# Kernel tuning notes

Measured on AMD Instinct MI355X. Metric: run time of the kernel, lower is better.

The kernel has to match this reference:

```python
import jax, jax.numpy as jnp
import numpy as np

ALPHA = 0.2  # LeakyReLU negative slope
NEG = -9e15  # mask value from original code


def setup_inputs() -> dict:
    key = jax.random.key(0)
    k1, k2, k3, k4 = jax.random.split(key, 4)
    N, F_in, F_out = 8192, 256, 128
    h = jax.random.normal(k1, (N, F_in), dtype=jnp.float32)
    adj = jax.random.randint(k2, (N, N), 0, 2, dtype=jnp.int32)
    # xavier-ish scaled params
    W = jax.random.normal(k3, (F_out, F_in), dtype=jnp.float32) * (1.0 / np.sqrt(F_in))
    a = jax.random.normal(k4, (1, 2 * F_out), dtype=jnp.float32) * (1.0 / np.sqrt(2 * F_out))
    return {"h": h, "adj": adj, "W": W, "a": a}


def reference(h, adj, W, a):
    # Wh: [N, F_out]
    Wh = h @ W.T
    F_out = Wh.shape[1]
    # Algebraic decomposition of the pairwise-concat score:
    # e[i,j] = leakyrelu(a . [Wh_i ; Wh_j]) = leakyrelu(f1_i + f2_j)
    a1 = a[0, :F_out]   # [F_out]
    a2 = a[0, F_out:]   # [F_out]
    f1 = Wh @ a1        # [N]
    f2 = Wh @ a2        # [N]
    e = jax.nn.leaky_relu(f1[:, None] + f2[None, :], negative_slope=ALPHA)  # [N, N]
    scores = jnp.where(adj > 0, e, NEG)
    attention = jax.nn.softmax(scores, axis=1)  # dropout omitted (eval mode)
    return attention @ Wh  # [N, F_out]
```

## Files before the change

### kernel.cpp

```cpp
#include <hip/hip_runtime.h>
#include <hip/hip_bf16.h>


typedef __bf16 bf16;
typedef __attribute__((ext_vector_type(8))) __bf16 bf16x8;
typedef __attribute__((ext_vector_type(4))) float f32x4;

#define NN 8192
#define F_IN 256
#define F_OUT 128
#define LOG2E 1.44269504088896f
#define ALPHA 0.2f
#define KSLICES 8

__device__ __forceinline__ void split8(const float* __restrict__ p,
                                       bf16x8& hi, bf16x8& lo) {
    const float4 u = *(const float4*)p;
    const float4 v = *(const float4*)(p + 4);
    float f[8] = {u.x, u.y, u.z, u.w, v.x, v.y, v.z, v.w};
#pragma unroll
    for (int j = 0; j < 8; ++j) {
        const bf16 h = (bf16)f[j];
        hi[j] = h;
        lo[j] = (bf16)(f[j] - (float)h);
    }
}

__global__ __launch_bounds__(256) void gat_whpack(
        const int* __restrict__ adj,
        const float* __restrict__ h,
        const float* __restrict__ W,
        const float* __restrict__ a,
        unsigned char* __restrict__ maskP,
        bf16* __restrict__ WhT,
        float* __restrict__ f1L,
        float* __restrict__ f2L) {
    const int tid = threadIdx.x;

    if (blockIdx.x < 2048) {
        const int row = blockIdx.x * 4 + (tid >> 6);
        const int l = tid & 63;
        const int* rowp = adj + (size_t)row * NN;

#pragma unroll 4
        for (int iter = 0; iter < 16; ++iter) {
            const int base = iter * 512;
            const int4 v1 = *(const int4*)(rowp + base + l * 4);
            const int4 v2 = *(const int4*)(rowp + base + 256 + l * 4);
            unsigned int n1 = (v1.x > 0 ? 1u : 0u) | (v1.y > 0 ? 2u : 0u) |
                              (v1.z > 0 ? 4u : 0u) | (v1.w > 0 ? 8u : 0u);
            unsigned int n2 = (v2.x > 0 ? 1u : 0u) | (v2.y > 0 ? 2u : 0u) |
                              (v2.z > 0 ? 4u : 0u) | (v2.w > 0 ? 8u : 0u);
            const unsigned int p1 = __shfl_xor(n1, 1);
            const unsigned int p2 = __shfl_xor(n2, 1);
            if ((l & 1) == 0) {
                const int b1 = iter * 64 + (l >> 1);
                const int b2 = b1 + 32;
                maskP[((size_t)(b1 >> 7) << 20) + (size_t)row * 128 + (b1 & 127)] =
                    (unsigned char)(n1 | (p1 << 4));
                maskP[((size_t)(b2 >> 7) << 20) + (size_t)row * 128 + (b2 & 127)] =
                    (unsigned char)(n2 | (p2 << 4));
            }
        }
        return;
    }

    const int wb = blockIdx.x - 2048;
    const int wv = tid >> 6;
    const int l15 = tid & 15;
    const int g = (tid & 63) >> 4;
    const int rowbase = wb * 64 + wv * 16;

    f32x4 acc[8];
    const f32x4 zz = {0.f, 0.f, 0.f, 0.f};
#pragma unroll
    for (int nf = 0; nf < 8; ++nf) acc[nf] = zz;

#pragma unroll
    for (int ks = 0; ks < 8; ++ks) {
        const int k = ks * 32 + g * 8;
        bf16x8 ah, al;
        split8(h + (size_t)(rowbase + l15) * F_IN + k, ah, al);
#pragma unroll
        for (int nf = 0; nf < 8; ++nf) {
            bf16x8 bh, bl;
            split8(W + (size_t)(nf * 16 + l15) * F_IN + k, bh, bl);
            acc[nf] = __builtin_amdgcn_mfma_f32_16x16x32_bf16(ah, bh, acc[nf], 0, 0, 0);
            acc[nf] = __builtin_amdgcn_mfma_f32_16x16x32_bf16(ah, bl, acc[nf], 0, 0, 0);
            acc[nf] = __builtin_amdgcn_mfma_f32_16x16x32_bf16(al, bh, acc[nf], 0, 0, 0);
        }
    }

#pragma unroll
    for (int nf = 0; nf < 8; ++nf)
#pragma unroll
        for (int r = 0; r < 4; ++r)
            WhT[(size_t)(nf * 16 + l15) * NN + rowbase + g * 4 + r] = (bf16)acc[nf][r];

    float a1c[8], a2c[8];
#pragma unroll
    for (int nf = 0; nf < 8; ++nf) {
        a1c[nf] = a[nf * 16 + l15];
        a2c[nf] = a[F_OUT + nf * 16 + l15];
    }
#pragma unroll
    for (int r = 0; r < 4; ++r) {
        float s1 = 0.f, s2 = 0.f;
#pragma unroll
        for (int nf = 0; nf < 8; ++nf) {
            s1 += acc[nf][r] * a1c[nf];
            s2 += acc[nf][r] * a2c[nf];
        }
        s1 += __shfl_xor(s1, 1, 16);
        s1 += __shfl_xor(s1, 2, 16);
        s1 += __shfl_xor(s1, 4, 16);
        s1 += __shfl_xor(s1, 8, 16);
        s2 += __shfl_xor(s2, 1, 16);
        s2 += __shfl_xor(s2, 2, 16);
        s2 += __shfl_xor(s2, 4, 16);
        s2 += __shfl_xor(s2, 8, 16);
        if (l15 == 0) {
            f1L[rowbase + g * 4 + r] = s1 * LOG2E;
            f2L[rowbase + g * 4 + r] = s2 * LOG2E;
        }
    }
}

__global__ __launch_bounds__(512, 4) void gat_flash6(
        const unsigned char* __restrict__ maskP,
        const bf16* __restrict__ WhT,
        const float* __restrict__ f1L,
        const float* __restrict__ f2L,
        float* __restrict__ O_part,
        float* __restrict__ rs_part) {
    __shared__ __align__(16) char lds[39424];

    const int tid = threadIdx.x;
    const int wv = tid >> 6;
    const int l = tid & 63;
    const int l15 = l & 15;
    const int g = l >> 4;
    const int rb = blockIdx.x >> 3;
    const int ks = blockIdx.x & 7;
    const int row0 = rb * 128;
    const int lrow = wv * 16 + l15;

    const float f1a = f1L[row0 + lrow];

    const int mr = tid >> 2;
    const int mseg = tid & 3;
    const unsigned char* msrc =
        maskP + ((size_t)ks << 20) + (size_t)(row0 + mr) * 128 + mseg * 4;

    f32x4 acc[8];
    const f32x4 zz = {0.f, 0.f, 0.f, 0.f};
#pragma unroll
    for (int nf = 0; nf < 8; ++nf) acc[nf] = zz;
    float rs0 = 0.f;

    {
        const float2 v = *(const float2*)(f2L + ks * 1024 + tid * 2);
        *(float2*)(lds + 35328 + tid * 8) = v;
    }

    for (int it = 0; it < 8; ++it) {
        __syncthreads();
        const unsigned int mw = *(const unsigned int*)(msrc + it * 16);
        *(unsigned int*)(lds + 32768 + mr * 20 + mseg * 4) = mw;
#pragma unroll
        for (int j = 0; j < 4; ++j) {
            const int u = j * 512 + tid;
            const int cc = u >> 4;
            const int ku = u & 15;
            const bf16x8 v =
                *(const bf16x8*)(WhT + (size_t)cc * NN + ks * 1024 + it * 128 + ku * 8);
            *(bf16x8*)(lds + ((cc * 256 + ku * 16) ^ ((cc & 7) << 4))) = v;
        }
        __syncthreads();

#pragma unroll
        for (int s = 0; s < 4; ++s) {
            const unsigned int mb =
                *(const unsigned char*)(lds + 32768 + lrow * 20 + s * 4 + g);
            const int t = it * 4 + s;
            const float4 fa = *(const float4*)(lds + 35328 + t * 128 + g * 32);
            const float4 fb = *(const float4*)(lds + 35328 + t * 128 + g * 32 + 16);
            const float ff[8] = {fa.x, fa.y, fa.z, fa.w, fb.x, fb.y, fb.z, fb.w};

            bf16x8 pa;
#pragma unroll
            for (int j = 0; j < 8; ++j) {
                const float x = f1a + ff[j];
                const float e = __builtin_amdgcn_exp2f(fmaxf(x, ALPHA * x));
                pa[j] = (bf16)((mb & (1u << j)) ? e : 0.f);
            }
#pragma unroll
            for (int j = 0; j < 8; ++j) rs0 += (float)pa[j];

            __builtin_amdgcn_s_setprio(1);
#pragma unroll
            for (int nf = 0; nf < 8; ++nf) {
                const int c = nf * 16 + l15;
                const bf16x8 bh = *(const bf16x8*)(
                    lds + ((c * 256 + s * 64 + g * 16) ^ ((c & 7) << 4)));
                acc[nf] = __builtin_amdgcn_mfma_f32_16x16x32_bf16(pa, bh, acc[nf], 0, 0, 0);
            }
            __builtin_amdgcn_s_setprio(0);
        }
    }

    rs0 += __shfl_xor(rs0, 16);
    rs0 += __shfl_xor(rs0, 32);
    if (l < 16) rs_part[(size_t)ks * NN + row0 + lrow] = rs0;

    float* accL = (float*)lds;
#pragma unroll
    for (int half = 0; half < 2; ++half) {
        __syncthreads();
        if ((wv >> 2) == half) {
            const int rbase = (wv & 3) * 16;
#pragma unroll
            for (int nf = 0; nf < 8; ++nf)
#pragma unroll
                for (int r = 0; r < 4; ++r)
                    accL[(rbase + g * 4 + r) * 132 + nf * 16 + l15] = acc[nf][r];
        }
        __syncthreads();
        const int rr = tid >> 3;
        const int seg = tid & 7;
        float* dst = O_part + ((size_t)ks << 20) +
                     (size_t)(row0 + half * 64 + rr) * F_OUT + seg * 16;
        const float* src = accL + rr * 132 + seg * 16;
        *(float4*)(dst + 0) = *(const float4*)(src + 0);
        *(float4*)(dst + 4) = *(const float4*)(src + 4);
        *(float4*)(dst + 8) = *(const float4*)(src + 8);
        *(float4*)(dst + 12) = *(const float4*)(src + 12);
    }
}

__global__ __launch_bounds__(256) void gat_reduce(const float* __restrict__ O_part,
                                                  const float* __restrict__ rs_part,
                                                  float* __restrict__ out) {
    const int idx = blockIdx.x * 256 + threadIdx.x;
    const int r = idx >> 5;
    const int c = (idx & 31) * 4;
    float rsum = 0.f;
#pragma unroll
    for (int s = 0; s < KSLICES; ++s) rsum += rs_part[(size_t)s * NN + r];
    float4 o = {0.f, 0.f, 0.f, 0.f};
#pragma unroll
    for (int s = 0; s < KSLICES; ++s) {
        const float4 v =
            *(const float4*)(O_part + ((size_t)s << 20) + (size_t)r * F_OUT + c);
        o.x += v.x;
        o.y += v.y;
        o.z += v.z;
        o.w += v.w;
    }
    const float inv = 1.0f / rsum;
    o.x *= inv;
    o.y *= inv;
    o.z *= inv;
    o.w *= inv;
    *(float4*)(out + (size_t)r * F_OUT + c) = o;
}

extern "C" void kernel_launch(void* const* d_in, const int* in_sizes, int n_in,
                              void* d_out, int out_size, void* d_ws, size_t ws_size,
                              hipStream_t stream) {
    const float* h = (const float*)d_in[0];
    const int* adj = (const int*)d_in[1];
    const float* W = (const float*)d_in[2];
    const float* a = (const float*)d_in[3];
    float* out = (float*)d_out;

    char* ws = (char*)d_ws;
    const size_t MB = 1024 * 1024;
    bf16* WhT = (bf16*)ws;
    float* f1L = (float*)(ws + 2 * MB);
    float* f2L = f1L + NN;
    unsigned char* maskP = (unsigned char*)(ws + 3 * MB);
    float* rs_part = (float*)(ws + 11 * MB);
    float* O_part = (float*)(ws + 12 * MB);

    gat_whpack<<<2176, 256, 0, stream>>>(adj, h, W, a, maskP, WhT, f1L, f2L);
    gat_flash6<<<512, 512, 0, stream>>>(maskP, WhT, f1L, f2L, O_part, rs_part);
    gat_reduce<<<NN * F_OUT / 4 / 256, 256, 0, stream>>>(O_part, rs_part, out);
}
```

Baseline: 131.4 us.

## Fuse split-K reduction into flash kernel with ordered per-row-block turn counters

Drops the separate reduce kernel. The K-slices of each row block now accumulate into one O buffer in sequence, coordinated by an atomic turn counter per row block, and the last slice normalizes and writes the output. The grid order is changed so slices run ks-major and earlier slices are scheduled first. The whpack kernel is reordered to place the Wh blocks first and to reset the counters. This removes one launch and the 8-way partial-buffer traffic, but adds spin-wait serialization across slices and relies on forward progress of earlier blocks.

Measured after the change: 365.0 us. 2.78x slower.

```diff
diff --git a/kernel.cpp b/kernel.cpp
--- a/kernel.cpp
+++ b/kernel.cpp
@@ -11,7 +11,6 @@
 #define F_OUT 128
 #define LOG2E 1.44269504088896f
 #define ALPHA 0.2f
-#define KSLICES 8
 
 __device__ __forceinline__ void split8(const float* __restrict__ p,
                                        bf16x8& hi, bf16x8& lo) {
@@ -34,11 +33,12 @@
         unsigned char* __restrict__ maskP,
         bf16* __restrict__ WhT,
         float* __restrict__ f1L,
-        float* __restrict__ f2L) {
+        float* __restrict__ f2L,
+        int* __restrict__ turn) {
     const int tid = threadIdx.x;
 
-    if (blockIdx.x < 2048) {
-        const int row = blockIdx.x * 4 + (tid >> 6);
+    if (blockIdx.x >= 128) {
+        const int row = (blockIdx.x - 128) * 4 + (tid >> 6);
         const int l = tid & 63;
         const int* rowp = adj + (size_t)row * NN;
 
@@ -65,7 +65,9 @@
         return;
     }
 
-    const int wb = blockIdx.x - 2048;
+    if (blockIdx.x == 0 && tid < 64) turn[tid] = 0;
+
+    const int wb = blockIdx.x;
     const int wv = tid >> 6;
     const int l15 = tid & 15;
     const int g = (tid & 63) >> 4;
@@ -126,13 +128,17 @@
     }
 }
 
-__global__ __launch_bounds__(512, 4) void gat_flash6(
+#define RSOFF 34048
+
+__global__ __launch_bounds__(512, 4) void gat_flash6t(
         const unsigned char* __restrict__ maskP,
         const bf16* __restrict__ WhT,
         const float* __restrict__ f1L,
         const float* __restrict__ f2L,
-        float* __restrict__ O_part,
-        float* __restrict__ rs_part) {
+        float* __restrict__ rs_part,
+        float* __restrict__ O_acc,
+        int* __restrict__ turn,
+        float* __restrict__ out) {
     __shared__ __align__(16) char lds[39424];
 
     const int tid = threadIdx.x;
@@ -140,8 +146,8 @@
     const int l = tid & 63;
     const int l15 = l & 15;
     const int g = l >> 4;
-    const int rb = blockIdx.x >> 3;
-    const int ks = blockIdx.x & 7;
+    const int ks = blockIdx.x >> 6;
+    const int rb = blockIdx.x & 63;
     const int row0 = rb * 128;
     const int lrow = wv * 16 + l15;
 
@@ -211,13 +217,36 @@
 
     rs0 += __shfl_xor(rs0, 16);
     rs0 += __shfl_xor(rs0, 32);
-    if (l < 16) rs_part[(size_t)ks * NN + row0 + lrow] = rs0;
+    if (l < 16) {
+        if (ks < 7)
+            rs_part[(size_t)ks * NN + row0 + lrow] = rs0;
+        else
+            *(float*)(lds + RSOFF + lrow * 4) = rs0;
+    }
+    __syncthreads();
+
+    if (tid == 0 && ks > 0) {
+        while (__hip_atomic_load(&turn[rb], __ATOMIC_ACQUIRE,
+                                 __HIP_MEMORY_SCOPE_AGENT) < ks)
+            __builtin_amdgcn_s_sleep(8);
+        __threadfence();
+    }
+    __syncthreads();
+
+    if (ks == 7 && tid < 128) {
+        float r = *(const float*)(lds + RSOFF + tid * 4);
+#pragma unroll
+        for (int s = 0; s < 7; ++s) r += rs_part[(size_t)s * NN + row0 + tid];
+        *(float*)(lds + RSOFF + 512 + tid * 4) = 1.0f / r;
+    }
 
     float* accL = (float*)lds;
-#pragma unroll
-    for (int half = 0; half < 2; ++half) {
+    float* O_blk = O_acc + (size_t)rb * (128 * 128);
+
+#pragma unroll
+    for (int hh = 0; hh < 2; ++hh) {
         __syncthreads();
-        if ((wv >> 2) == half) {
+        if ((wv >> 2) == hh) {
             const int rbase = (wv & 3) * 16;
 #pragma unroll
             for (int nf = 0; nf < 8; ++nf)
@@ -228,41 +257,43 @@
         __syncthreads();
         const int rr = tid >> 3;
         const int seg = tid & 7;
-        float* dst = O_part + ((size_t)ks << 20) +
-                     (size_t)(row0 + half * 64 + rr) * F_OUT + seg * 16;
         const float* src = accL + rr * 132 + seg * 16;
-        *(float4*)(dst + 0) = *(const float4*)(src + 0);
-        *(float4*)(dst + 4) = *(const float4*)(src + 4);
-        *(float4*)(dst + 8) = *(const float4*)(src + 8);
-        *(float4*)(dst + 12) = *(const float4*)(src + 12);
-    }
-}
-
-__global__ __launch_bounds__(256) void gat_reduce(const float* __restrict__ O_part,
-                                                  const float* __restrict__ rs_part,
-                                                  float* __restrict__ out) {
-    const int idx = blockIdx.x * 256 + threadIdx.x;
-    const int r = idx >> 5;
-    const int c = (idx & 31) * 4;
-    float rsum = 0.f;
-#pragma unroll
-    for (int s = 0; s < KSLICES; ++s) rsum += rs_part[(size_t)s * NN + r];
-    float4 o = {0.f, 0.f, 0.f, 0.f};
-#pragma unroll
-    for (int s = 0; s < KSLICES; ++s) {
-        const float4 v =
-            *(const float4*)(O_part + ((size_t)s << 20) + (size_t)r * F_OUT + c);
-        o.x += v.x;
-        o.y += v.y;
-        o.z += v.z;
-        o.w += v.w;
-    }
-    const float inv = 1.0f / rsum;
-    o.x *= inv;
-    o.y *= inv;
-    o.z *= inv;
-    o.w *= inv;
-    *(float4*)(out + (size_t)r * F_OUT + c) = o;
+        const int grow = hh * 64 + rr;
+        if (ks == 0) {
+            float* dst = O_blk + (size_t)grow * 128 + seg * 16;
+#pragma unroll
+            for (int j = 0; j < 4; ++j)
+                *(float4*)(dst + j * 4) = *(const float4*)(src + j * 4);
+        } else if (ks < 7) {
+            float* dst = O_blk + (size_t)grow * 128 + seg * 16;
+#pragma unroll
+            for (int j = 0; j < 4; ++j) {
+                float4 v = *(const float4*)(dst + j * 4);
+                const float4 u = *(const float4*)(src + j * 4);
+                v.x += u.x; v.y += u.y; v.z += u.z; v.w += u.w;
+                *(float4*)(dst + j * 4) = v;
+            }
+        } else {
+            const float inv = *(const float*)(lds + RSOFF + 512 + grow * 4);
+            const float* osrc = O_blk + (size_t)grow * 128 + seg * 16;
+            float* dst = out + (size_t)(row0 + grow) * F_OUT + seg * 16;
+#pragma unroll
+            for (int j = 0; j < 4; ++j) {
+                float4 v = *(const float4*)(osrc + j * 4);
+                const float4 u = *(const float4*)(src + j * 4);
+                v.x = (v.x + u.x) * inv; v.y = (v.y + u.y) * inv;
+                v.z = (v.z + u.z) * inv; v.w = (v.w + u.w) * inv;
+                *(float4*)(dst + j * 4) = v;
+            }
+        }
+    }
+
+    __syncthreads();
+    if (tid == 0 && ks < 7) {
+        __threadfence();
+        __hip_atomic_store(&turn[rb], ks + 1, __ATOMIC_RELEASE,
+                           __HIP_MEMORY_SCOPE_AGENT);
+    }
 }
 
 extern "C" void kernel_launch(void* const* d_in, const int* in_sizes, int n_in,
@@ -279,11 +310,11 @@
     bf16* WhT = (bf16*)ws;
     float* f1L = (float*)(ws + 2 * MB);
     float* f2L = f1L + NN;
+    int* turn = (int*)(ws + 2 * MB + 64 * 1024);
     unsigned char* maskP = (unsigned char*)(ws + 3 * MB);
     float* rs_part = (float*)(ws + 11 * MB);
-    float* O_part = (float*)(ws + 12 * MB);
-
-    gat_whpack<<<2176, 256, 0, stream>>>(adj, h, W, a, maskP, WhT, f1L, f2L);
-    gat_flash6<<<512, 512, 0, stream>>>(maskP, WhT, f1L, f2L, O_part, rs_part);
-    gat_reduce<<<NN * F_OUT / 4 / 256, 256, 0, stream>>>(O_part, rs_part, out);
+    float* O_acc = (float*)(ws + 12 * MB);
+
+    gat_whpack<<<2176, 256, 0, stream>>>(adj, h, W, a, maskP, WhT, f1L, f2L, turn);
+    gat_flash6t<<<512, 512, 0, stream>>>(maskP, WhT, f1L, f2L, rs_part, O_acc, turn, out);
 }
```
